# Performance work log

Measured on AMD Instinct MI355X. Metric: run time of the kernel, lower is better.

## Reference

```python
import jax, jax.numpy as jnp
from jax import lax
import numpy as np

B, H, W, C = 8, 192, 192, 64   # decoder feature map at crop_layer 0 (NHWC)
N = 1024                       # total detections across the batch (flattened ragged)
S = 32                         # crop_size
NCLS = 3                       # n_cls
CH = 64                        # conv_channels


def setup_inputs() -> dict:
    key = jax.random.key(0)
    ks = jax.random.split(key, 12)
    features = jax.random.normal(ks[0], (B, H, W, C), jnp.float32)
    # normalized [y1, x1, y2, x2] boxes, well-formed and inside the image
    cy = jax.random.uniform(ks[1], (N,), minval=0.2, maxval=0.8)
    cx = jax.random.uniform(ks[2], (N,), minval=0.2, maxval=0.8)
    sy = jax.random.uniform(ks[3], (N,), minval=0.05, maxval=0.3)
    sx = jax.random.uniform(ks[4], (N,), minval=0.05, maxval=0.3)
    boxes = jnp.stack([
        jnp.clip(cy - sy / 2, 0.0, 1.0),
        jnp.clip(cx - sx / 2, 0.0, 1.0),
        jnp.clip(cy + sy / 2, 0.0, 1.0),
        jnp.clip(cx + sx / 2, 0.0, 1.0),
    ], axis=-1).astype(jnp.float32)
    box_ids = jax.random.randint(ks[5], (N,), 0, B, dtype=jnp.int32)
    cls = jax.random.randint(ks[6], (N,), 0, NCLS, dtype=jnp.int32)
    scale = 0.05
    conv1_w = jax.random.normal(ks[7], (3, 3, C, CH), jnp.float32) * scale
    conv1_b = jnp.zeros((CH,), jnp.float32)
    conv2_w = jax.random.normal(ks[8], (3, 3, CH, CH), jnp.float32) * scale
    conv2_b = jnp.zeros((CH,), jnp.float32)
    out_w = jax.random.normal(ks[9], (3, 3, CH, NCLS), jnp.float32) * scale
    out_b = jnp.zeros((NCLS,), jnp.float32)
    return dict(features=features, boxes=boxes, box_ids=box_ids, cls=cls,
                conv1_w=conv1_w, conv1_b=conv1_b, conv2_w=conv2_w, conv2_b=conv2_b,
                out_w=out_w, out_b=out_b)


def _crop_and_resize(features, boxes, box_ids, size):
    """tf.image.crop_and_resize-style bilinear per-box crop. -> [N, size, size, C]"""
    Hh, Ww = features.shape[1], features.shape[2]
    y1, x1, y2, x2 = boxes[:, 0], boxes[:, 1], boxes[:, 2], boxes[:, 3]
    t = jnp.arange(size, dtype=features.dtype) / (size - 1)
    ys = (y1[:, None] + t[None, :] * (y2 - y1)[:, None]) * (Hh - 1)  # [N,S]
    xs = (x1[:, None] + t[None, :] * (x2 - x1)[:, None]) * (Ww - 1)  # [N,S]
    y0 = jnp.clip(jnp.floor(ys), 0, Hh - 1)
    x0 = jnp.clip(jnp.floor(xs), 0, Ww - 1)
    wy = (ys - y0)[:, :, None, None]   # [N,S,1,1]
    wx = (xs - x0)[:, None, :, None]   # [N,1,S,1]
    y0i = y0.astype(jnp.int32); x0i = x0.astype(jnp.int32)
    y1i = jnp.minimum(y0i + 1, Hh - 1); x1i = jnp.minimum(x0i + 1, Ww - 1)
    b = box_ids[:, None, None]
    def g(yi, xi):  # gather [N,S,S,C]
        return features[b, yi[:, :, None], xi[:, None, :]]
    v00, v01 = g(y0i, x0i), g(y0i, x1i)
    v10, v11 = g(y1i, x0i), g(y1i, x1i)
    top = v00 * (1 - wx) + v01 * wx
    bot = v10 * (1 - wx) + v11 * wx
    return top * (1 - wy) + bot * wy


def _conv(x, w, b, pad):
    return lax.conv_general_dilated(x, w, (1, 1), pad,
                                    dimension_numbers=('NHWC', 'HWIO', 'NHWC')) + b


def reference(features, boxes, box_ids, cls, conv1_w, conv1_b, conv2_w, conv2_b, out_w, out_b):
    x = _crop_and_resize(features, boxes, box_ids, S)            # [N,32,32,C]
    x = jax.nn.relu(_conv(x, conv1_w, conv1_b, 'SAME'))          # mask_conv1
    x = jax.nn.relu(_conv(x, conv2_w, conv2_b, 'SAME'))          # mask_conv1 (second)
    m = _conv(x, out_w, out_b, 'VALID')                          # [N,30,30,n_cls]
    # batched class-channel gather: tf.gather(masks, cls[:,None], axis=-1, batch_dims=1)
    masks = m[jnp.arange(m.shape[0]), :, :, cls][..., None]      # [N,30,30,1]
    return masks
```

## Files before the change

kernel.cpp:

```cpp
#include <hip/hip_runtime.h>

#define HH 192
#define WW 192
#define CC 64
#define NB 1024
#define SS 32

typedef __bf16 bf16x8 __attribute__((ext_vector_type(8)));
typedef float  f32x4  __attribute__((ext_vector_type(4)));

__device__ __forceinline__ unsigned short f2bf(float f) {
    unsigned int u = __builtin_bit_cast(unsigned int, f);
    u += 0x7FFFu + ((u >> 16) & 1u);
    return (unsigned short)(u >> 16);
}

__global__ __launch_bounds__(256) void wprep_kernel(
        const float* __restrict__ c1w, const float* __restrict__ c2w,
        const float* __restrict__ ow, unsigned short* __restrict__ wt1,
        unsigned short* __restrict__ wt2, unsigned short* __restrict__ wto) {
    int b = blockIdx.x;
    if (b < 288) {
        const float* w = (b < 144) ? c1w : c2w;
        unsigned short* wt = (b < 144) ? wt1 : wt2;
        int idx = (b < 144 ? b : b - 144) * 256 + threadIdx.x;
        int j    = idx & 7;
        int lane = (idx >> 3) & 63;
        int nt   = (idx >> 9) & 3;
        int kc   = (idx >> 11) & 1;
        int tap  = idx >> 12;
        int c = kc * 32 + ((lane >> 4) << 3) + j;
        int o = (nt << 4) + (lane & 15);
        wt[idx] = f2bf(w[(tap * 64 + c) * 64 + o]);
    } else {
        int idx = (b - 288) * 256 + threadIdx.x;
        int j    = idx & 7;
        int lane = (idx >> 3) & 63;
        int kc   = (idx >> 9) & 1;
        int tap  = idx >> 10;
        int c = kc * 32 + ((lane >> 4) << 3) + j;
        int o = lane & 15;
        wto[idx] = (o < 3) ? f2bf(ow[(tap * 64 + c) * 3 + o]) : (unsigned short)0;
    }
}

__global__ __launch_bounds__(256, 3) void crop_conv1_kernel(
        const float* __restrict__ feat, const float* __restrict__ boxes,
        const int* __restrict__ box_ids, const unsigned short* __restrict__ wt,
        const float* __restrict__ bias, unsigned short* __restrict__ out, int n0) {
    __shared__ unsigned short s_in[10 * 32 * 72];

    int nl = blockIdx.y;
    int gn = n0 + nl;
    int y0 = blockIdx.x << 3;
    int t = threadIdx.x;
    int wave = t >> 6, lane = t & 63;
    int quad = lane >> 4, mcol = lane & 15;

    {
        int px = t >> 3, cg = t & 7, c0 = cg << 3;
        float by1 = boxes[gn * 4 + 0];
        float bx1 = boxes[gn * 4 + 1];
        float by2 = boxes[gn * 4 + 2];
        float bx2 = boxes[gn * 4 + 3];
        float tx = (float)px / 31.0f;
        float xs = (bx1 + tx * (bx2 - bx1)) * 191.0f;
        float x0f = fminf(fmaxf(floorf(xs), 0.0f), 191.0f);
        float wx = xs - x0f;
        int x0i = (int)x0f, x1i = min(x0i + 1, 191);
        const float* fb = feat + (size_t)box_ids[gn] * (HH * WW * CC);
        unsigned short* dst = s_in + px * 72 + c0;
#pragma unroll 2
        for (int r = 0; r < 10; r++) {
            int gy = y0 + r - 1;
            uint4 v = {0, 0, 0, 0};
            if (gy >= 0 && gy < 32) {
                float ty = (float)gy / 31.0f;
                float ys = (by1 + ty * (by2 - by1)) * 191.0f;
                float y0f = fminf(fmaxf(floorf(ys), 0.0f), 191.0f);
                float wy = ys - y0f;
                int y0i = (int)y0f, y1i = min(y0i + 1, 191);
                const float* p00 = fb + ((size_t)y0i * WW + x0i) * CC + c0;
                const float* p01 = fb + ((size_t)y0i * WW + x1i) * CC + c0;
                const float* p10 = fb + ((size_t)y1i * WW + x0i) * CC + c0;
                const float* p11 = fb + ((size_t)y1i * WW + x1i) * CC + c0;
                unsigned int rr[4];
#pragma unroll
                for (int h = 0; h < 2; h++) {
                    float4 v00 = *(const float4*)(p00 + 4 * h);
                    float4 v01 = *(const float4*)(p01 + 4 * h);
                    float4 v10 = *(const float4*)(p10 + 4 * h);
                    float4 v11 = *(const float4*)(p11 + 4 * h);
                    const float* a00 = (const float*)&v00;
                    const float* a01 = (const float*)&v01;
                    const float* a10 = (const float*)&v10;
                    const float* a11 = (const float*)&v11;
#pragma unroll
                    for (int i = 0; i < 4; i++) {
                        float top = a00[i] + wx * (a01[i] - a00[i]);
                        float bot = a10[i] + wx * (a11[i] - a10[i]);
                        float val = top + wy * (bot - top);
                        unsigned short bb = f2bf(val);
                        int e = 4 * h + i;
                        if (e & 1) rr[e >> 1] |= ((unsigned int)bb << 16);
                        else       rr[e >> 1]  = (unsigned int)bb;
                    }
                }
                v = *(uint4*)rr;
            }
            *(uint4*)(dst + r * 32 * 72) = v;
        }
    }
    __syncthreads();

    f32x4 acc[4][4];
#pragma unroll
    for (int nt = 0; nt < 4; nt++) {
        float bv = bias[(nt << 4) + mcol];
#pragma unroll
        for (int mi = 0; mi < 4; mi++) acc[mi][nt] = (f32x4){bv, bv, bv, bv};
    }

    int r0 = wave << 1;
#pragma unroll
    for (int dy = 0; dy < 3; dy++) {
#pragma unroll
        for (int dx = 0; dx < 3; dx++) {
            int tap = dy * 3 + dx;
#pragma unroll
            for (int kc = 0; kc < 2; kc++) {
                uint4 bfr[4];
#pragma unroll
                for (int nt = 0; nt < 4; nt++)
                    bfr[nt] = *(const uint4*)(wt + ((((tap * 2 + kc) * 4 + nt) * 64 + lane) << 3));
                uint4 afr[4];
#pragma unroll
                for (int mi = 0; mi < 4; mi++) {
                    int xs = ((mi & 1) << 4) + mcol + dx - 1;
                    uint4 a = {0, 0, 0, 0};
                    if (xs >= 0 && xs < 32)
                        a = *(const uint4*)(s_in + ((r0 + (mi >> 1) + dy) * 32 + xs) * 72 +
                                            (kc << 5) + (quad << 3));
                    afr[mi] = a;
                }
#pragma unroll
                for (int mi = 0; mi < 4; mi++)
#pragma unroll
                    for (int nt = 0; nt < 4; nt++)
                        acc[mi][nt] = __builtin_amdgcn_mfma_f32_16x16x32_bf16(
                            __builtin_bit_cast(bf16x8, afr[mi]),
                            __builtin_bit_cast(bf16x8, bfr[nt]), acc[mi][nt], 0, 0, 0);
            }
        }
    }

#pragma unroll
    for (int mi = 0; mi < 4; mi++) {
        int yy = y0 + r0 + (mi >> 1);
        int xb = ((mi & 1) << 4) + (quad << 2);
#pragma unroll
        for (int reg = 0; reg < 4; reg++) {
            unsigned short* op = out + (((size_t)nl * 32 + yy) * 32 + (xb + reg)) * 64 + mcol;
#pragma unroll
            for (int nt = 0; nt < 4; nt++) {
                float v = fmaxf(acc[mi][nt][reg], 0.0f);
                op[nt << 4] = f2bf(v);
            }
        }
    }
}

#define S_IN_ELEMS (12 * 32 * 64)
__global__ __launch_bounds__(256, 2) void conv2_out_kernel(
        const unsigned short* __restrict__ in, const unsigned short* __restrict__ wt,
        const float* __restrict__ bias, const unsigned short* __restrict__ wto,
        const float* __restrict__ ob, const int* __restrict__ cls,
        float* __restrict__ out, int n0) {
    __shared__ unsigned short s_in[S_IN_ELEMS + 4096];

    int nl = blockIdx.y;
    int y0 = blockIdx.x << 3;
    int t = threadIdx.x;
    int wave = t >> 6, lane = t & 63;
    int quad = lane >> 4, mcol = lane & 15;

    {
        int px = t >> 3, cg = t & 7;
        const unsigned short* src = in + (((size_t)nl * 32) * 32 + px) * 64 + (cg << 3);
        unsigned short* dst = s_in + (px << 6) + ((cg ^ (px & 7)) << 3);
#pragma unroll
        for (int r = 0; r < 12; r++) {
            int gy = y0 + r - 1;
            uint4 v = {0, 0, 0, 0};
            if (gy >= 0 && gy < 32) v = *(const uint4*)(src + (size_t)gy * 2048);
            *(uint4*)(dst + (r << 11)) = v;
        }
    }
    __syncthreads();

    float bv[4];
#pragma unroll
    for (int nt = 0; nt < 4; nt++) bv[nt] = bias[(nt << 4) + mcol];

    f32x4 acc[5][4];
#pragma unroll
    for (int i = 0; i < 5; i++)
#pragma unroll
        for (int nt = 0; nt < 4; nt++)
            acc[i][nt] = (f32x4){bv[nt], bv[nt], bv[nt], bv[nt]};

    int mt0 = wave * 5;
#pragma unroll
    for (int dy = 0; dy < 3; dy++) {
#pragma unroll
        for (int dx = 0; dx < 3; dx++) {
            int tap = dy * 3 + dx;
#pragma unroll
            for (int kc = 0; kc < 2; kc++) {
                int cslot = (kc << 2) + quad;
                uint4 bfr[4];
#pragma unroll
                for (int nt = 0; nt < 4; nt++)
                    bfr[nt] = *(const uint4*)(wt + ((((tap * 2 + kc) * 4 + nt) * 64 + lane) << 3));
#pragma unroll
                for (int i = 0; i < 5; i++) {
                    int mt = mt0 + i;
                    int lr = mt >> 1, h = mt & 1;
                    int xs = (h << 4) + mcol + dx - 1;
                    uint4 a = {0, 0, 0, 0};
                    if (xs >= 0 && xs < 32)
                        a = *(const uint4*)(s_in + (((lr + dy) * 32 + xs) << 6) +
                                            ((cslot ^ (xs & 7)) << 3));
#pragma unroll
                    for (int nt = 0; nt < 4; nt++)
                        acc[i][nt] = __builtin_amdgcn_mfma_f32_16x16x32_bf16(
                            __builtin_bit_cast(bf16x8, a),
                            __builtin_bit_cast(bf16x8, bfr[nt]), acc[i][nt], 0, 0, 0);
                }
            }
        }
    }
    __syncthreads();

#pragma unroll
    for (int i = 0; i < 5; i++) {
        int mt = mt0 + i;
        int lr = mt >> 1, h = mt & 1;
        int xb = (h << 4) + (quad << 2);
#pragma unroll
        for (int reg = 0; reg < 4; reg++) {
            int px = xb + reg;
#pragma unroll
            for (int nt = 0; nt < 4; nt++) {
                int oc = (nt << 4) + mcol;
                float v = fmaxf(acc[i][nt][reg], 0.0f);
                s_in[((lr * 32 + px) << 6) + (((oc >> 3) ^ (px & 7)) << 3) + (oc & 7)] = f2bf(v);
            }
        }
    }
    __syncthreads();

    f32x4 acc2[4];
#pragma unroll
    for (int mi = 0; mi < 4; mi++) acc2[mi] = (f32x4){0.f, 0.f, 0.f, 0.f};

    int r0 = wave << 1;
#pragma unroll
    for (int dy = 0; dy < 3; dy++) {
#pragma unroll
        for (int dx = 0; dx < 3; dx++) {
            int tap = dy * 3 + dx;
#pragma unroll
            for (int kc = 0; kc < 2; kc++) {
                int cslot = (kc << 2) + quad;
                uint4 bfr = *(const uint4*)(wto + (((tap * 2 + kc) * 64 + lane) << 3));
#pragma unroll
                for (int mi = 0; mi < 4; mi++) {
                    int xs = ((mi & 1) << 4) + mcol + dx;
                    if (xs > 31) xs = 31;
                    uint4 a = *(const uint4*)(s_in + (((r0 + (mi >> 1) + dy) * 32 + xs) << 6) +
                                              ((cslot ^ (xs & 7)) << 3));
                    acc2[mi] = __builtin_amdgcn_mfma_f32_16x16x32_bf16(
                        __builtin_bit_cast(bf16x8, a),
                        __builtin_bit_cast(bf16x8, bfr), acc2[mi], 0, 0, 0);
                }
            }
        }
    }

    int gn = n0 + nl;
    int oc = cls[gn];
    if (mcol == oc) {
        float obv = ob[oc];
#pragma unroll
        for (int mi = 0; mi < 4; mi++) {
            int yy = y0 + r0 + (mi >> 1);
            int xb = ((mi & 1) << 4) + (quad << 2);
            if (yy < 30) {
#pragma unroll
                for (int reg = 0; reg < 4; reg++) {
                    int x = xb + reg;
                    if (x < 30)
                        out[(size_t)gn * 900 + yy * 30 + x] = acc2[mi][reg] + obv;
                }
            }
        }
    }
}

extern "C" void kernel_launch(void* const* d_in, const int* in_sizes, int n_in,
                              void* d_out, int out_size, void* d_ws, size_t ws_size,
                              hipStream_t stream) {
    const float* feat    = (const float*)d_in[0];
    const float* boxes   = (const float*)d_in[1];
    const int*   box_ids = (const int*)d_in[2];
    const int*   cls     = (const int*)d_in[3];
    const float* c1w     = (const float*)d_in[4];
    const float* c1b     = (const float*)d_in[5];
    const float* c2w     = (const float*)d_in[6];
    const float* c2b     = (const float*)d_in[7];
    const float* ow      = (const float*)d_in[8];
    const float* ob      = (const float*)d_in[9];

    unsigned short* wt1  = (unsigned short*)d_ws;
    unsigned short* wt2  = wt1 + 36864;
    unsigned short* wto  = wt2 + 36864;
    unsigned short* bufA = wto + 9216;

    size_t wt_bytes = (size_t)(36864 * 2 + 9216) * 2;
    size_t avail = (ws_size > wt_bytes) ? (ws_size - wt_bytes) : 0;
    size_t per_box = (size_t)32 * 32 * 64 * 2;
    int nc = (int)(avail / per_box);
    if (nc >= 512) nc = 512;
    else {
        int p = 1;
        while (p * 2 <= nc) p *= 2;
        nc = (p < 1) ? 1 : p;
    }

    wprep_kernel<<<324, 256, 0, stream>>>(c1w, c2w, ow, wt1, wt2, wto);

    for (int nn0 = 0; nn0 < NB; nn0 += nc) {
        int cur = (NB - nn0 < nc) ? (NB - nn0) : nc;
        crop_conv1_kernel<<<dim3(4, cur), 256, 0, stream>>>(feat, boxes, box_ids,
                                                            wt1, c1b, bufA, nn0);
        conv2_out_kernel<<<dim3(4, cur), 256, 0, stream>>>(bufA, wt2, c2b, wto, ob,
                                                           cls, (float*)d_out, nn0);
    }
}
```

Before: 374.3 us.

## Fuse crop, conv1, conv2 and output conv into one kernel with halo recompute

Replaces the two-kernel pipeline (crop+conv1 writing a bf16 intermediate to global, then conv2+out conv) with a single 512-thread kernel per (row-block, box). Each block crops a 14-row halo, computes conv1 on 12 rows and conv2 on 10 rows in shared memory, then applies the output conv. This removes the global round trip of the conv1 activations and the chunked launches. In exchange it recomputes conv1 halo rows (about 50% extra conv1 work) and uses more shared memory per block, which may limit occupancy.

```diff
diff --git a/kernel.cpp b/kernel.cpp
--- a/kernel.cpp
+++ b/kernel.cpp
@@ -44,41 +44,45 @@
     }
 }
 
-__global__ __launch_bounds__(256, 3) void crop_conv1_kernel(
+__global__ __launch_bounds__(512, 2) void mega_kernel(
         const float* __restrict__ feat, const float* __restrict__ boxes,
-        const int* __restrict__ box_ids, const unsigned short* __restrict__ wt,
-        const float* __restrict__ bias, unsigned short* __restrict__ out, int n0) {
-    __shared__ unsigned short s_in[10 * 32 * 72];
-
-    int nl = blockIdx.y;
-    int gn = n0 + nl;
+        const int* __restrict__ box_ids,
+        const unsigned short* __restrict__ wt1, const float* __restrict__ c1b,
+        const unsigned short* __restrict__ wt2, const float* __restrict__ c2b,
+        const unsigned short* __restrict__ wto, const float* __restrict__ ob,
+        const int* __restrict__ cls, float* __restrict__ out) {
+    __shared__ unsigned short s_crop[14 * 32 * 64];
+    __shared__ unsigned short s_c1[12 * 32 * 64];
+
+    int gn = blockIdx.y;
     int y0 = blockIdx.x << 3;
     int t = threadIdx.x;
     int wave = t >> 6, lane = t & 63;
     int quad = lane >> 4, mcol = lane & 15;
 
     {
-        int px = t >> 3, cg = t & 7, c0 = cg << 3;
+        int px = (t >> 3) & 31, cg = t & 7, sub = t >> 8, c0 = cg << 3;
         float by1 = boxes[gn * 4 + 0];
         float bx1 = boxes[gn * 4 + 1];
         float by2 = boxes[gn * 4 + 2];
         float bx2 = boxes[gn * 4 + 3];
         float tx = (float)px / 31.0f;
-        float xs = (bx1 + tx * (bx2 - bx1)) * 191.0f;
-        float x0f = fminf(fmaxf(floorf(xs), 0.0f), 191.0f);
-        float wx = xs - x0f;
+        float xsf = (bx1 + tx * (bx2 - bx1)) * 191.0f;
+        float x0f = fminf(fmaxf(floorf(xsf), 0.0f), 191.0f);
+        float wx = xsf - x0f;
         int x0i = (int)x0f, x1i = min(x0i + 1, 191);
         const float* fb = feat + (size_t)box_ids[gn] * (HH * WW * CC);
-        unsigned short* dst = s_in + px * 72 + c0;
+        unsigned short* dst = s_crop + (px << 6) + ((cg ^ (px & 7)) << 3);
 #pragma unroll 2
-        for (int r = 0; r < 10; r++) {
-            int gy = y0 + r - 1;
+        for (int i = 0; i < 7; i++) {
+            int r = sub * 7 + i;
+            int gy = y0 - 2 + r;
             uint4 v = {0, 0, 0, 0};
             if (gy >= 0 && gy < 32) {
                 float ty = (float)gy / 31.0f;
-                float ys = (by1 + ty * (by2 - by1)) * 191.0f;
-                float y0f = fminf(fmaxf(floorf(ys), 0.0f), 191.0f);
-                float wy = ys - y0f;
+                float ysf = (by1 + ty * (by2 - by1)) * 191.0f;
+                float y0f = fminf(fmaxf(floorf(ysf), 0.0f), 191.0f);
+                float wy = ysf - y0f;
                 int y0i = (int)y0f, y1i = min(y0i + 1, 191);
                 const float* p00 = fb + ((size_t)y0i * WW + x0i) * CC + c0;
                 const float* p01 = fb + ((size_t)y0i * WW + x1i) * CC + c0;
@@ -96,212 +100,181 @@
                     const float* a10 = (const float*)&v10;
                     const float* a11 = (const float*)&v11;
 #pragma unroll
-                    for (int i = 0; i < 4; i++) {
-                        float top = a00[i] + wx * (a01[i] - a00[i]);
-                        float bot = a10[i] + wx * (a11[i] - a10[i]);
+                    for (int e2 = 0; e2 < 4; e2++) {
+                        float top = a00[e2] + wx * (a01[e2] - a00[e2]);
+                        float bot = a10[e2] + wx * (a11[e2] - a10[e2]);
                         float val = top + wy * (bot - top);
                         unsigned short bb = f2bf(val);
-                        int e = 4 * h + i;
+                        int e = 4 * h + e2;
                         if (e & 1) rr[e >> 1] |= ((unsigned int)bb << 16);
                         else       rr[e >> 1]  = (unsigned int)bb;
                     }
                 }
                 v = *(uint4*)rr;
             }
-            *(uint4*)(dst + r * 32 * 72) = v;
+            *(uint4*)(dst + (r << 11)) = v;
         }
     }
     __syncthreads();
 
-    f32x4 acc[4][4];
-#pragma unroll
-    for (int nt = 0; nt < 4; nt++) {
-        float bv = bias[(nt << 4) + mcol];
-#pragma unroll
-        for (int mi = 0; mi < 4; mi++) acc[mi][nt] = (f32x4){bv, bv, bv, bv};
-    }
-
-    int r0 = wave << 1;
-#pragma unroll
-    for (int dy = 0; dy < 3; dy++) {
-#pragma unroll
-        for (int dx = 0; dx < 3; dx++) {
-            int tap = dy * 3 + dx;
-#pragma unroll
-            for (int kc = 0; kc < 2; kc++) {
-                uint4 bfr[4];
-#pragma unroll
-                for (int nt = 0; nt < 4; nt++)
-                    bfr[nt] = *(const uint4*)(wt + ((((tap * 2 + kc) * 4 + nt) * 64 + lane) << 3));
-                uint4 afr[4];
-#pragma unroll
-                for (int mi = 0; mi < 4; mi++) {
-                    int xs = ((mi & 1) << 4) + mcol + dx - 1;
-                    uint4 a = {0, 0, 0, 0};
-                    if (xs >= 0 && xs < 32)
-                        a = *(const uint4*)(s_in + ((r0 + (mi >> 1) + dy) * 32 + xs) * 72 +
-                                            (kc << 5) + (quad << 3));
-                    afr[mi] = a;
-                }
-#pragma unroll
-                for (int mi = 0; mi < 4; mi++)
+    {
+        f32x4 acc1[3][4];
+#pragma unroll
+        for (int i = 0; i < 3; i++)
+#pragma unroll
+            for (int nt = 0; nt < 4; nt++) {
+                float bv = c1b[(nt << 4) + mcol];
+                acc1[i][nt] = (f32x4){bv, bv, bv, bv};
+            }
+#pragma unroll
+        for (int dy = 0; dy < 3; dy++) {
+#pragma unroll
+            for (int dx = 0; dx < 3; dx++) {
+                int tap = dy * 3 + dx;
+#pragma unroll
+                for (int kc = 0; kc < 2; kc++) {
+                    int cslot = (kc << 2) + quad;
+                    uint4 bfr[4];
 #pragma unroll
                     for (int nt = 0; nt < 4; nt++)
-                        acc[mi][nt] = __builtin_amdgcn_mfma_f32_16x16x32_bf16(
-                            __builtin_bit_cast(bf16x8, afr[mi]),
-                            __builtin_bit_cast(bf16x8, bfr[nt]), acc[mi][nt], 0, 0, 0);
-            }
-        }
-    }
-
-#pragma unroll
-    for (int mi = 0; mi < 4; mi++) {
-        int yy = y0 + r0 + (mi >> 1);
-        int xb = ((mi & 1) << 4) + (quad << 2);
-#pragma unroll
-        for (int reg = 0; reg < 4; reg++) {
-            unsigned short* op = out + (((size_t)nl * 32 + yy) * 32 + (xb + reg)) * 64 + mcol;
+                        bfr[nt] = *(const uint4*)(wt1 + ((((tap * 2 + kc) * 4 + nt) * 64 + lane) << 3));
+#pragma unroll
+                    for (int i = 0; i < 3; i++) {
+                        int mt = wave * 3 + i;
+                        int lr1 = mt >> 1, h = mt & 1;
+                        int xs = (h << 4) + mcol + dx - 1;
+                        uint4 a = {0, 0, 0, 0};
+                        if (xs >= 0 && xs < 32)
+                            a = *(const uint4*)(s_crop + (((lr1 + dy) * 32 + xs) << 6) +
+                                                ((cslot ^ (xs & 7)) << 3));
+#pragma unroll
+                        for (int nt = 0; nt < 4; nt++)
+                            acc1[i][nt] = __builtin_amdgcn_mfma_f32_16x16x32_bf16(
+                                __builtin_bit_cast(bf16x8, a),
+                                __builtin_bit_cast(bf16x8, bfr[nt]), acc1[i][nt], 0, 0, 0);
+                    }
+                }
+            }
+        }
+#pragma unroll
+        for (int i = 0; i < 3; i++) {
+            int mt = wave * 3 + i;
+            int lr1 = mt >> 1, h = mt & 1;
+            int g1 = y0 - 1 + lr1;
+            bool ok = (g1 >= 0 && g1 < 32);
+#pragma unroll
+            for (int reg = 0; reg < 4; reg++) {
+                int px = (h << 4) + (quad << 2) + reg;
+#pragma unroll
+                for (int nt = 0; nt < 4; nt++) {
+                    int oc = (nt << 4) + mcol;
+                    float v = ok ? fmaxf(acc1[i][nt][reg], 0.0f) : 0.0f;
+                    s_c1[((lr1 * 32 + px) << 6) + (((oc >> 3) ^ (px & 7)) << 3) + (oc & 7)] = f2bf(v);
+                }
+            }
+        }
+    }
+    __syncthreads();
+
+    {
+        f32x4 acc2[3][4];
+#pragma unroll
+        for (int i = 0; i < 3; i++)
 #pragma unroll
             for (int nt = 0; nt < 4; nt++) {
-                float v = fmaxf(acc[mi][nt][reg], 0.0f);
-                op[nt << 4] = f2bf(v);
-            }
-        }
-    }
-}
-
-#define S_IN_ELEMS (12 * 32 * 64)
-__global__ __launch_bounds__(256, 2) void conv2_out_kernel(
-        const unsigned short* __restrict__ in, const unsigned short* __restrict__ wt,
-        const float* __restrict__ bias, const unsigned short* __restrict__ wto,
-        const float* __restrict__ ob, const int* __restrict__ cls,
-        float* __restrict__ out, int n0) {
-    __shared__ unsigned short s_in[S_IN_ELEMS + 4096];
-
-    int nl = blockIdx.y;
-    int y0 = blockIdx.x << 3;
-    int t = threadIdx.x;
-    int wave = t >> 6, lane = t & 63;
-    int quad = lane >> 4, mcol = lane & 15;
+                float bv = c2b[(nt << 4) + mcol];
+                acc2[i][nt] = (f32x4){bv, bv, bv, bv};
+            }
+#pragma unroll
+        for (int dy = 0; dy < 3; dy++) {
+#pragma unroll
+            for (int dx = 0; dx < 3; dx++) {
+                int tap = dy * 3 + dx;
+#pragma unroll
+                for (int kc = 0; kc < 2; kc++) {
+                    int cslot = (kc << 2) + quad;
+                    uint4 bfr[4];
+#pragma unroll
+                    for (int nt = 0; nt < 4; nt++)
+                        bfr[nt] = *(const uint4*)(wt2 + ((((tap * 2 + kc) * 4 + nt) * 64 + lane) << 3));
+#pragma unroll
+                    for (int i = 0; i < 3; i++) {
+                        int mt = wave + (i << 3);
+                        if (mt < 20) {
+                            int lr2 = mt >> 1, h = mt & 1;
+                            int xs = (h << 4) + mcol + dx - 1;
+                            uint4 a = {0, 0, 0, 0};
+                            if (xs >= 0 && xs < 32)
+                                a = *(const uint4*)(s_c1 + (((lr2 + dy) * 32 + xs) << 6) +
+                                                    ((cslot ^ (xs & 7)) << 3));
+#pragma unroll
+                            for (int nt = 0; nt < 4; nt++)
+                                acc2[i][nt] = __builtin_amdgcn_mfma_f32_16x16x32_bf16(
+                                    __builtin_bit_cast(bf16x8, a),
+                                    __builtin_bit_cast(bf16x8, bfr[nt]), acc2[i][nt], 0, 0, 0);
+                        }
+                    }
+                }
+            }
+        }
+#pragma unroll
+        for (int i = 0; i < 3; i++) {
+            int mt = wave + (i << 3);
+            if (mt < 20) {
+                int lr2 = mt >> 1, h = mt & 1;
+#pragma unroll
+                for (int reg = 0; reg < 4; reg++) {
+                    int px = (h << 4) + (quad << 2) + reg;
+#pragma unroll
+                    for (int nt = 0; nt < 4; nt++) {
+                        int oc = (nt << 4) + mcol;
+                        float v = fmaxf(acc2[i][nt][reg], 0.0f);
+                        s_crop[((lr2 * 32 + px) << 6) + (((oc >> 3) ^ (px & 7)) << 3) + (oc & 7)] = f2bf(v);
+                    }
+                }
+            }
+        }
+    }
+    __syncthreads();
 
     {
-        int px = t >> 3, cg = t & 7;
-        const unsigned short* src = in + (((size_t)nl * 32) * 32 + px) * 64 + (cg << 3);
-        unsigned short* dst = s_in + (px << 6) + ((cg ^ (px & 7)) << 3);
-#pragma unroll
-        for (int r = 0; r < 12; r++) {
-            int gy = y0 + r - 1;
-            uint4 v = {0, 0, 0, 0};
-            if (gy >= 0 && gy < 32) v = *(const uint4*)(src + (size_t)gy * 2048);
-            *(uint4*)(dst + (r << 11)) = v;
-        }
-    }
-    __syncthreads();
-
-    float bv[4];
-#pragma unroll
-    for (int nt = 0; nt < 4; nt++) bv[nt] = bias[(nt << 4) + mcol];
-
-    f32x4 acc[5][4];
-#pragma unroll
-    for (int i = 0; i < 5; i++)
-#pragma unroll
-        for (int nt = 0; nt < 4; nt++)
-            acc[i][nt] = (f32x4){bv[nt], bv[nt], bv[nt], bv[nt]};
-
-    int mt0 = wave * 5;
-#pragma unroll
-    for (int dy = 0; dy < 3; dy++) {
-#pragma unroll
-        for (int dx = 0; dx < 3; dx++) {
-            int tap = dy * 3 + dx;
-#pragma unroll
-            for (int kc = 0; kc < 2; kc++) {
-                int cslot = (kc << 2) + quad;
-                uint4 bfr[4];
-#pragma unroll
-                for (int nt = 0; nt < 4; nt++)
-                    bfr[nt] = *(const uint4*)(wt + ((((tap * 2 + kc) * 4 + nt) * 64 + lane) << 3));
-#pragma unroll
-                for (int i = 0; i < 5; i++) {
-                    int mt = mt0 + i;
-                    int lr = mt >> 1, h = mt & 1;
-                    int xs = (h << 4) + mcol + dx - 1;
-                    uint4 a = {0, 0, 0, 0};
-                    if (xs >= 0 && xs < 32)
-                        a = *(const uint4*)(s_in + (((lr + dy) * 32 + xs) << 6) +
-                                            ((cslot ^ (xs & 7)) << 3));
-#pragma unroll
-                    for (int nt = 0; nt < 4; nt++)
-                        acc[i][nt] = __builtin_amdgcn_mfma_f32_16x16x32_bf16(
+        f32x4 acc3[2];
+        acc3[0] = (f32x4){0.f, 0.f, 0.f, 0.f};
+        acc3[1] = (f32x4){0.f, 0.f, 0.f, 0.f};
+#pragma unroll
+        for (int dy = 0; dy < 3; dy++) {
+#pragma unroll
+            for (int dx = 0; dx < 3; dx++) {
+                int tap = dy * 3 + dx;
+#pragma unroll
+                for (int kc = 0; kc < 2; kc++) {
+                    int cslot = (kc << 2) + quad;
+                    uint4 bfr = *(const uint4*)(wto + (((tap * 2 + kc) * 64 + lane) << 3));
+#pragma unroll
+                    for (int mi = 0; mi < 2; mi++) {
+                        int xs = (mi << 4) + mcol + dx;
+                        if (xs > 31) xs = 31;
+                        uint4 a = *(const uint4*)(s_crop + (((wave + dy) * 32 + xs) << 6) +
+                                                  ((cslot ^ (xs & 7)) << 3));
+                        acc3[mi] = __builtin_amdgcn_mfma_f32_16x16x32_bf16(
                             __builtin_bit_cast(bf16x8, a),
-                            __builtin_bit_cast(bf16x8, bfr[nt]), acc[i][nt], 0, 0, 0);
-                }
-            }
-        }
-    }
-    __syncthreads();
-
-#pragma unroll
-    for (int i = 0; i < 5; i++) {
-        int mt = mt0 + i;
-        int lr = mt >> 1, h = mt & 1;
-        int xb = (h << 4) + (quad << 2);
-#pragma unroll
-        for (int reg = 0; reg < 4; reg++) {
-            int px = xb + reg;
-#pragma unroll
-            for (int nt = 0; nt < 4; nt++) {
-                int oc = (nt << 4) + mcol;
-                float v = fmaxf(acc[i][nt][reg], 0.0f);
-                s_in[((lr * 32 + px) << 6) + (((oc >> 3) ^ (px & 7)) << 3) + (oc & 7)] = f2bf(v);
-            }
-        }
-    }
-    __syncthreads();
-
-    f32x4 acc2[4];
-#pragma unroll
-    for (int mi = 0; mi < 4; mi++) acc2[mi] = (f32x4){0.f, 0.f, 0.f, 0.f};
-
-    int r0 = wave << 1;
-#pragma unroll
-    for (int dy = 0; dy < 3; dy++) {
-#pragma unroll
-        for (int dx = 0; dx < 3; dx++) {
-            int tap = dy * 3 + dx;
-#pragma unroll
-            for (int kc = 0; kc < 2; kc++) {
-                int cslot = (kc << 2) + quad;
-                uint4 bfr = *(const uint4*)(wto + (((tap * 2 + kc) * 64 + lane) << 3));
-#pragma unroll
-                for (int mi = 0; mi < 4; mi++) {
-                    int xs = ((mi & 1) << 4) + mcol + dx;
-                    if (xs > 31) xs = 31;
-                    uint4 a = *(const uint4*)(s_in + (((r0 + (mi >> 1) + dy) * 32 + xs) << 6) +
-                                              ((cslot ^ (xs & 7)) << 3));
-                    acc2[mi] = __builtin_amdgcn_mfma_f32_16x16x32_bf16(
-                        __builtin_bit_cast(bf16x8, a),
-                        __builtin_bit_cast(bf16x8, bfr), acc2[mi], 0, 0, 0);
-                }
-            }
-        }
-    }
-
-    int gn = n0 + nl;
-    int oc = cls[gn];
-    if (mcol == oc) {
-        float obv = ob[oc];
-#pragma unroll
-        for (int mi = 0; mi < 4; mi++) {
-            int yy = y0 + r0 + (mi >> 1);
-            int xb = ((mi & 1) << 4) + (quad << 2);
-            if (yy < 30) {
+                            __builtin_bit_cast(bf16x8, bfr), acc3[mi], 0, 0, 0);
+                    }
+                }
+            }
+        }
+        int oc = cls[gn];
+        int yy = y0 + wave;
+        if (mcol == oc && yy < 30) {
+            float obv = ob[oc];
+#pragma unroll
+            for (int mi = 0; mi < 2; mi++) {
+                int xb = (mi << 4) + (quad << 2);
 #pragma unroll
                 for (int reg = 0; reg < 4; reg++) {
                     int x = xb + reg;
                     if (x < 30)
-                        out[(size_t)gn * 900 + yy * 30 + x] = acc2[mi][reg] + obv;
+                        out[(size_t)gn * 900 + yy * 30 + x] = acc3[mi][reg] + obv;
                 }
             }
         }
@@ -325,26 +298,9 @@
     unsigned short* wt1  = (unsigned short*)d_ws;
     unsigned short* wt2  = wt1 + 36864;
     unsigned short* wto  = wt2 + 36864;
-    unsigned short* bufA = wto + 9216;
-
-    size_t wt_bytes = (size_t)(36864 * 2 + 9216) * 2;
-    size_t avail = (ws_size > wt_bytes) ? (ws_size - wt_bytes) : 0;
-    size_t per_box = (size_t)32 * 32 * 64 * 2;
-    int nc = (int)(avail / per_box);
-    if (nc >= 512) nc = 512;
-    else {
-        int p = 1;
-        while (p * 2 <= nc) p *= 2;
-        nc = (p < 1) ? 1 : p;
-    }
 
     wprep_kernel<<<324, 256, 0, stream>>>(c1w, c2w, ow, wt1, wt2, wto);
-
-    for (int nn0 = 0; nn0 < NB; nn0 += nc) {
-        int cur = (NB - nn0 < nc) ? (NB - nn0) : nc;
-        crop_conv1_kernel<<<dim3(4, cur), 256, 0, stream>>>(feat, boxes, box_ids,
-                                                            wt1, c1b, bufA, nn0);
-        conv2_out_kernel<<<dim3(4, cur), 256, 0, stream>>>(bufA, wt2, c2b, wto, ob,
-                                                           cls, (float*)d_out, nn0);
-    }
+    mega_kernel<<<dim3(4, NB), 512, 0, stream>>>(feat, boxes, box_ids,
+                                                 wt1, c1b, wt2, c2b, wto, ob,
+                                                 cls, (float*)d_out);
 }
```

Result: slower. 465.2 us (+24.3%).
